# Kernel optimization log

Measured on AMD Instinct MI355X. Metric: run time of the kernel, lower is better.

The kernel has to match this reference:

```python
import jax, jax.numpy as jnp
import numpy as np

B, C, T, F = 16, 2, 2000, 257

def setup_inputs() -> dict:
    key = jax.random.key(0)
    k1, = jax.random.split(key, 1)
    inp = jax.random.normal(k1, (B, C, T, F, 2), dtype=jnp.float32)
    s_1 = jnp.zeros((B, 1, F, 1), dtype=jnp.float32)
    weights = jnp.ones((1, C, 1, F, 1), dtype=jnp.float32)
    bias = jnp.zeros((1, C, 1, F, 1), dtype=jnp.float32)
    alpha_param = jnp.full((1, 1, F, 1), -4.0, dtype=jnp.float32)
    return {"input": inp, "s_1": s_1, "weights": weights, "bias": bias, "alpha_param": alpha_param}

def reference(input, s_1, weights, bias, alpha_param):
    # input: [B, C, T, F, 2]
    in_data2 = jnp.sum(input ** 2, axis=-1, keepdims=True)       # [B, C, T, F, 1]
    alpha = jax.nn.sigmoid(alpha_param)                           # [1, 1, F, 1]
    x_seq = jnp.moveaxis(in_data2[:, 0:1], 2, 0)                  # [T, B, 1, F, 1]

    def step(s, xt):
        s_new = s * (1.0 - alpha) + xt * alpha                    # [B, 1, F, 1]
        return s_new, s_new

    s_final, smooth = jax.lax.scan(step, s_1, x_seq)              # smooth: [T, B, 1, F, 1]
    smooth_data = jnp.sqrt(jnp.moveaxis(smooth, 0, 2))            # [B, 1, T, F, 1]
    cat_data = jnp.concatenate([smooth_data, jnp.sqrt(in_data2[:, 1:])], axis=1)  # [B, C, T, F, 1]
    res = input / (cat_data + 1e-8) * weights + bias              # [B, C, T, F, 2]
    return res, s_final, smooth_data
```

## Files before the change

kernel.cpp:

```cpp
#include <hip/hip_runtime.h>
#include <math.h>

#define B 16
#define C 2
#define T 2000
#define F 257
#define NC 50
#define L  (T / NC)

#define RES_SIZE   (B * C * T * F * 2)
#define OFF_SFINAL (RES_SIZE)
#define OFF_SMOOTH (RES_SIZE + B * F)

__device__ __forceinline__ float sigmoidf_(float x) {
    return 1.0f / (1.0f + expf(-x));
}

__global__ void k_carries(const float* __restrict__ input,
                          const float* __restrict__ alpha_param,
                          float* __restrict__ carry) {
    int tid = blockIdx.x * blockDim.x + threadIdx.x;
    const int N = B * F * NC;
    if (tid >= N) return;
    int f = tid % F;
    int r = tid / F;
    int c = r % NC;
    int b = r / NC;

    float a = sigmoidf_(alpha_param[f]);
    float beta = 1.0f - a;

    const float2* inp = (const float2*)input + ((size_t)(b * C + 0) * T + (size_t)c * L) * F + f;
    float s = 0.0f;
#pragma unroll 8
    for (int t = 0; t < L; ++t) {
        float2 v = inp[(size_t)t * F];
        float x = v.x * v.x + v.y * v.y;
        s = beta * s + a * x;
    }
    carry[(b * NC + c) * F + f] = s;
}

__global__ void k_scan(const float* __restrict__ s_1,
                       const float* __restrict__ alpha_param,
                       const float* __restrict__ carry,
                       float* __restrict__ chunkstart,
                       float* __restrict__ out) {
    int tid = blockIdx.x * blockDim.x + threadIdx.x;
    const int N = B * F;
    if (tid >= N) return;
    int f = tid % F;
    int b = tid / F;

    float a = sigmoidf_(alpha_param[f]);
    float beta = 1.0f - a;
    float bL = 1.0f;
#pragma unroll
    for (int i = 0; i < L; ++i) bL *= beta;

    float s = s_1[b * F + f];
    for (int c = 0; c < NC; ++c) {
        int idx = (b * NC + c) * F + f;
        chunkstart[idx] = s;
        s = bL * s + carry[idx];
    }
    out[OFF_SFINAL + b * F + f] = s;
}

__global__ void k_final0(const float* __restrict__ input,
                         const float* __restrict__ alpha_param,
                         const float* __restrict__ weights,
                         const float* __restrict__ bias,
                         const float* __restrict__ chunkstart,
                         float* __restrict__ out) {
    int tid = blockIdx.x * blockDim.x + threadIdx.x;
    const int N = B * F * NC;
    if (tid >= N) return;
    int f = tid % F;
    int r = tid / F;
    int c = r % NC;
    int b = r / NC;

    float a = sigmoidf_(alpha_param[f]);
    float beta = 1.0f - a;
    float w0 = weights[0 * F + f];
    float b0 = bias[0 * F + f];

    const float2* inp = (const float2*)input + ((size_t)(b * C + 0) * T + (size_t)c * L) * F + f;
    float2* res = (float2*)out + ((size_t)(b * C + 0) * T + (size_t)c * L) * F + f;
    float* smooth = out + OFF_SMOOTH + ((size_t)b * T + (size_t)c * L) * F + f;

    float s = chunkstart[(b * NC + c) * F + f];
#pragma unroll 8
    for (int t = 0; t < L; ++t) {
        float2 v = inp[(size_t)t * F];
        float x = v.x * v.x + v.y * v.y;
        s = beta * s + a * x;
        float sm = sqrtf(s);
        float inv = 1.0f / (sm + 1e-8f);
        float2 rr;
        rr.x = v.x * inv * w0 + b0;
        rr.y = v.y * inv * w0 + b0;
        res[(size_t)t * F] = rr;
        smooth[(size_t)t * F] = sm;
    }
}

__global__ void k_final1(const float* __restrict__ input,
                         const float* __restrict__ weights,
                         const float* __restrict__ bias,
                         float* __restrict__ out) {
    int tid = blockIdx.x * blockDim.x + threadIdx.x;
    const int N = B * T * F;
    if (tid >= N) return;
    int f = tid % F;
    int r = tid / F;
    int t = r % T;
    int b = r / T;

    float w1 = weights[1 * F + f];
    float b1 = bias[1 * F + f];

    const float2* inp = (const float2*)input + ((size_t)(b * C + 1) * T + t) * F + f;
    float2* res = (float2*)out + ((size_t)(b * C + 1) * T + t) * F + f;

    float2 v = *inp;
    float x = v.x * v.x + v.y * v.y;
    float sm = sqrtf(x);
    float inv = 1.0f / (sm + 1e-8f);
    float2 rr;
    rr.x = v.x * inv * w1 + b1;
    rr.y = v.y * inv * w1 + b1;
    *res = rr;
}

extern "C" void kernel_launch(void* const* d_in, const int* in_sizes, int n_in,
                              void* d_out, int out_size, void* d_ws, size_t ws_size,
                              hipStream_t stream) {
    const float* input       = (const float*)d_in[0];
    const float* s_1         = (const float*)d_in[1];
    const float* weights     = (const float*)d_in[2];
    const float* bias        = (const float*)d_in[3];
    const float* alpha_param = (const float*)d_in[4];
    float* out = (float*)d_out;

    float* carry      = (float*)d_ws;
    float* chunkstart = (float*)d_ws + B * NC * F;

    const int N1 = B * F * NC;
    const int N2 = B * F;
    const int N3 = B * T * F;

    k_carries<<<(N1 + 255) / 256, 256, 0, stream>>>(input, alpha_param, carry);
    k_scan<<<(N2 + 255) / 256, 256, 0, stream>>>(s_1, alpha_param, carry, chunkstart, out);
    k_final0<<<(N1 + 255) / 256, 256, 0, stream>>>(input, alpha_param, weights, bias, chunkstart, out);
    k_final1<<<(N3 + 255) / 256, 256, 0, stream>>>(input, weights, bias, out);
}
```

Baseline: 303.0 us.

## Fuse scan stages and channel-1 normalization into one kernel with inter-block flags

```diff
diff --git a/kernel.cpp b/kernel.cpp
--- a/kernel.cpp
+++ b/kernel.cpp
@@ -12,126 +12,154 @@
 #define OFF_SFINAL (RES_SIZE)
 #define OFF_SMOOTH (RES_SIZE + B * F)
 
+#define NCHUNK_BLOCKS (B * NC)
+#define NCH1_BLOCKS   1200
+#define BLOCK_DIM     320
+
+#define CH1_F4_PER_B  257000
+#define CH1_F4_TOTAL  (B * CH1_F4_PER_B)
+
 __device__ __forceinline__ float sigmoidf_(float x) {
     return 1.0f / (1.0f + expf(-x));
 }
 
-__global__ void k_carries(const float* __restrict__ input,
-                          const float* __restrict__ alpha_param,
-                          float* __restrict__ carry) {
-    int tid = blockIdx.x * blockDim.x + threadIdx.x;
-    const int N = B * F * NC;
-    if (tid >= N) return;
-    int f = tid % F;
-    int r = tid / F;
-    int c = r % NC;
-    int b = r / NC;
+__global__ __launch_bounds__(BLOCK_DIM) void fused_kernel(
+        const float* __restrict__ input,
+        const float* __restrict__ s_1,
+        const float* __restrict__ weights,
+        const float* __restrict__ bias,
+        const float* __restrict__ alpha_param,
+        float* __restrict__ out,
+        int* __restrict__ cnt,
+        int* __restrict__ scanflag,
+        float* __restrict__ carries,
+        float* __restrict__ chunkstart)
+{
+    const int bid = blockIdx.x;
 
-    float a = sigmoidf_(alpha_param[f]);
-    float beta = 1.0f - a;
+    if (bid < NCHUNK_BLOCKS) {
+        const int b = bid % B;
+        const int c = bid / B;
+        const int f = threadIdx.x;
+        const bool active = (f < F);
 
-    const float2* inp = (const float2*)input + ((size_t)(b * C + 0) * T + (size_t)c * L) * F + f;
-    float s = 0.0f;
-#pragma unroll 8
-    for (int t = 0; t < L; ++t) {
-        float2 v = inp[(size_t)t * F];
-        float x = v.x * v.x + v.y * v.y;
-        s = beta * s + a * x;
+        float a = 0.f, beta = 0.f;
+        if (active) {
+            a = sigmoidf_(alpha_param[f]);
+            beta = 1.0f - a;
+        }
+
+        const float2* inp = (const float2*)input + ((size_t)(b * C + 0) * T + (size_t)c * L) * F + f;
+
+        if (active) {
+            float s = 0.0f;
+#pragma unroll 4
+            for (int t = 0; t < L; ++t) {
+                float2 v = inp[(size_t)t * F];
+                float x = v.x * v.x + v.y * v.y;
+                s = beta * s + a * x;
+            }
+            __hip_atomic_store(&carries[(b * NC + c) * F + f], s,
+                               __ATOMIC_RELAXED, __HIP_MEMORY_SCOPE_AGENT);
+        }
+        __syncthreads();
+        if (threadIdx.x == 0) {
+            __threadfence();
+            atomicAdd(&cnt[b], 1);
+        }
+
+        if (c == 0) {
+            if (threadIdx.x == 0) {
+                while (__hip_atomic_load(&cnt[b], __ATOMIC_RELAXED, __HIP_MEMORY_SCOPE_AGENT) < NC) {
+                    __builtin_amdgcn_s_sleep(2);
+                }
+            }
+            __syncthreads();
+            __threadfence();
+            if (active) {
+                float bL = 1.0f;
+#pragma unroll
+                for (int i = 0; i < L; ++i) bL *= beta;
+                float s = s_1[b * F + f];
+                for (int c2 = 0; c2 < NC; ++c2) {
+                    __hip_atomic_store(&chunkstart[(b * NC + c2) * F + f], s,
+                                       __ATOMIC_RELAXED, __HIP_MEMORY_SCOPE_AGENT);
+                    float cr = __hip_atomic_load(&carries[(b * NC + c2) * F + f],
+                                                 __ATOMIC_RELAXED, __HIP_MEMORY_SCOPE_AGENT);
+                    s = bL * s + cr;
+                }
+                out[OFF_SFINAL + b * F + f] = s;
+            }
+            __syncthreads();
+            if (threadIdx.x == 0) {
+                __threadfence();
+                __hip_atomic_store(&scanflag[b], 1, __ATOMIC_RELAXED, __HIP_MEMORY_SCOPE_AGENT);
+            }
+        } else {
+            if (threadIdx.x == 0) {
+                while (__hip_atomic_load(&scanflag[b], __ATOMIC_RELAXED, __HIP_MEMORY_SCOPE_AGENT) == 0) {
+                    __builtin_amdgcn_s_sleep(2);
+                }
+            }
+            __syncthreads();
+            __threadfence();
+        }
+
+        if (active) {
+            const float w0 = weights[0 * F + f];
+            const float b0 = bias[0 * F + f];
+            float s = __hip_atomic_load(&chunkstart[(b * NC + c) * F + f],
+                                        __ATOMIC_RELAXED, __HIP_MEMORY_SCOPE_AGENT);
+            float2* res = (float2*)out + ((size_t)(b * C + 0) * T + (size_t)c * L) * F + f;
+            float* smooth = out + OFF_SMOOTH + ((size_t)b * T + (size_t)c * L) * F + f;
+#pragma unroll 4
+            for (int t = 0; t < L; ++t) {
+                float2 v = inp[(size_t)t * F];
+                float x = v.x * v.x + v.y * v.y;
+                s = beta * s + a * x;
+                float sm = sqrtf(s);
+                float inv = 1.0f / (sm + 1e-8f);
+                float2 rr;
+                rr.x = v.x * inv * w0 + b0;
+                rr.y = v.y * inv * w0 + b0;
+                res[(size_t)t * F] = rr;
+                smooth[(size_t)t * F] = sm;
+            }
+        }
+    } else {
+        const int bid2 = bid - NCHUNK_BLOCKS;
+        const int stride = NCH1_BLOCKS * BLOCK_DIM;
+        const float4* in4 = (const float4*)input;
+        float4* out4 = (float4*)out;
+
+        for (int w = bid2 * BLOCK_DIM + threadIdx.x; w < CH1_F4_TOTAL; w += stride) {
+            int b = w / CH1_F4_PER_B;
+            int r = w - b * CH1_F4_PER_B;
+            size_t f4idx = (size_t)CH1_F4_PER_B * (b * 2 + 1) + r;
+
+            float4 v = in4[f4idx];
+            int e0 = 2 * r;
+            int f0 = e0 % F;
+            int f1 = f0 + 1; if (f1 == F) f1 = 0;
+
+            float w1a = weights[F + f0], b1a = bias[F + f0];
+            float w1b = weights[F + f1], b1b = bias[F + f1];
+
+            float x0 = v.x * v.x + v.y * v.y;
+            float sm0 = sqrtf(x0);
+            float inv0 = 1.0f / (sm0 + 1e-8f);
+            float x1 = v.z * v.z + v.w * v.w;
+            float sm1 = sqrtf(x1);
+            float inv1 = 1.0f / (sm1 + 1e-8f);
+
+            float4 rr;
+            rr.x = v.x * inv0 * w1a + b1a;
+            rr.y = v.y * inv0 * w1a + b1a;
+            rr.z = v.z * inv1 * w1b + b1b;
+            rr.w = v.w * inv1 * w1b + b1b;
+            out4[f4idx] = rr;
+        }
     }
-    carry[(b * NC + c) * F + f] = s;
-}
-
-__global__ void k_scan(const float* __restrict__ s_1,
-                       const float* __restrict__ alpha_param,
-                       const float* __restrict__ carry,
-                       float* __restrict__ chunkstart,
-                       float* __restrict__ out) {
-    int tid = blockIdx.x * blockDim.x + threadIdx.x;
-    const int N = B * F;
-    if (tid >= N) return;
-    int f = tid % F;
-    int b = tid / F;
-
-    float a = sigmoidf_(alpha_param[f]);
-    float beta = 1.0f - a;
-    float bL = 1.0f;
-#pragma unroll
-    for (int i = 0; i < L; ++i) bL *= beta;
-
-    float s = s_1[b * F + f];
-    for (int c = 0; c < NC; ++c) {
-        int idx = (b * NC + c) * F + f;
-        chunkstart[idx] = s;
-        s = bL * s + carry[idx];
-    }
-    out[OFF_SFINAL + b * F + f] = s;
-}
-
-__global__ void k_final0(const float* __restrict__ input,
-                         const float* __restrict__ alpha_param,
-                         const float* __restrict__ weights,
-                         const float* __restrict__ bias,
-                         const float* __restrict__ chunkstart,
-                         float* __restrict__ out) {
-    int tid = blockIdx.x * blockDim.x + threadIdx.x;
-    const int N = B * F * NC;
-    if (tid >= N) return;
-    int f = tid % F;
-    int r = tid / F;
-    int c = r % NC;
-    int b = r / NC;
-
-    float a = sigmoidf_(alpha_param[f]);
-    float beta = 1.0f - a;
-    float w0 = weights[0 * F + f];
-    float b0 = bias[0 * F + f];
-
-    const float2* inp = (const float2*)input + ((size_t)(b * C + 0) * T + (size_t)c * L) * F + f;
-    float2* res = (float2*)out + ((size_t)(b * C + 0) * T + (size_t)c * L) * F + f;
-    float* smooth = out + OFF_SMOOTH + ((size_t)b * T + (size_t)c * L) * F + f;
-
-    float s = chunkstart[(b * NC + c) * F + f];
-#pragma unroll 8
-    for (int t = 0; t < L; ++t) {
-        float2 v = inp[(size_t)t * F];
-        float x = v.x * v.x + v.y * v.y;
-        s = beta * s + a * x;
-        float sm = sqrtf(s);
-        float inv = 1.0f / (sm + 1e-8f);
-        float2 rr;
-        rr.x = v.x * inv * w0 + b0;
-        rr.y = v.y * inv * w0 + b0;
-        res[(size_t)t * F] = rr;
-        smooth[(size_t)t * F] = sm;
-    }
-}
-
-__global__ void k_final1(const float* __restrict__ input,
-                         const float* __restrict__ weights,
-                         const float* __restrict__ bias,
-                         float* __restrict__ out) {
-    int tid = blockIdx.x * blockDim.x + threadIdx.x;
-    const int N = B * T * F;
-    if (tid >= N) return;
-    int f = tid % F;
-    int r = tid / F;
-    int t = r % T;
-    int b = r / T;
-
-    float w1 = weights[1 * F + f];
-    float b1 = bias[1 * F + f];
-
-    const float2* inp = (const float2*)input + ((size_t)(b * C + 1) * T + t) * F + f;
-    float2* res = (float2*)out + ((size_t)(b * C + 1) * T + t) * F + f;
-
-    float2 v = *inp;
-    float x = v.x * v.x + v.y * v.y;
-    float sm = sqrtf(x);
-    float inv = 1.0f / (sm + 1e-8f);
-    float2 rr;
-    rr.x = v.x * inv * w1 + b1;
-    rr.y = v.y * inv * w1 + b1;
-    *res = rr;
 }
 
 extern "C" void kernel_launch(void* const* d_in, const int* in_sizes, int n_in,
@@ -144,15 +172,15 @@
     const float* alpha_param = (const float*)d_in[4];
     float* out = (float*)d_out;
 
-    float* carry      = (float*)d_ws;
-    float* chunkstart = (float*)d_ws + B * NC * F;
+    int*   cnt        = (int*)d_ws;
+    int*   scanflag   = cnt + B;
+    float* carries    = (float*)d_ws + 32;
+    float* chunkstart = carries + B * NC * F;
 
-    const int N1 = B * F * NC;
-    const int N2 = B * F;
-    const int N3 = B * T * F;
+    hipMemsetAsync(d_ws, 0, 32 * sizeof(int), stream);
 
-    k_carries<<<(N1 + 255) / 256, 256, 0, stream>>>(input, alpha_param, carry);
-    k_scan<<<(N2 + 255) / 256, 256, 0, stream>>>(s_1, alpha_param, carry, chunkstart, out);
-    k_final0<<<(N1 + 255) / 256, 256, 0, stream>>>(input, alpha_param, weights, bias, chunkstart, out);
-    k_final1<<<(N3 + 255) / 256, 256, 0, stream>>>(input, weights, bias, out);
+    const int grid = NCHUNK_BLOCKS + NCH1_BLOCKS;
+    fused_kernel<<<grid, BLOCK_DIM, 0, stream>>>(
+        input, s_1, weights, bias, alpha_param, out,
+        cnt, scanflag, carries, chunkstart);
 }
```

Measured after the change: 447.0 us. +47.5%, slower.
